# Optimization experiments

Measured on AMD Instinct MI355X. Metric: run time of the kernel, lower is better.

## Reference

```python
import jax, jax.numpy as jnp
import numpy as np

FIELD = 39
VOCAB = 100000
EMB = 32
H1, H2 = 32, 32
BATCH = 16384


def setup_inputs() -> dict:
    key = jax.random.key(0)
    ks = jax.random.split(key, 10)
    Xi = jax.random.randint(ks[0], (BATCH, FIELD, 1), 0, VOCAB, dtype=jnp.int64 if jax.config.read('jax_enable_x64') else jnp.int32)
    Xv = jax.random.uniform(ks[1], (BATCH, FIELD), dtype=jnp.float32)
    # stacked per-field embedding tables (ModuleList of nn.Embedding)
    W1 = jax.random.normal(ks[2], (FIELD, VOCAB, 1), dtype=jnp.float32) * 0.01   # first-order
    W2 = jax.random.normal(ks[3], (FIELD, VOCAB, EMB), dtype=jnp.float32) * 0.01 # second-order
    # deep MLP params (torch Linear: y = x @ W.T + b; stored here as [in, out])
    lin1_w = jax.random.normal(ks[4], (FIELD * EMB, H1), dtype=jnp.float32) * (1.0 / np.sqrt(FIELD * EMB))
    lin1_b = jax.random.normal(ks[5], (H1,), dtype=jnp.float32) * 0.01
    lin2_w = jax.random.normal(ks[6], (H1, H2), dtype=jnp.float32) * (1.0 / np.sqrt(H1))
    lin2_b = jax.random.normal(ks[7], (H2,), dtype=jnp.float32) * 0.01
    bias = jax.random.normal(ks[8], (1,), dtype=jnp.float32)
    return {"Xi": Xi, "Xv": Xv, "W1": W1, "W2": W2, "lin1_w": lin1_w,
            "lin1_b": lin1_b, "lin2_w": lin2_w, "lin2_b": lin2_b, "bias": bias}


def reference(Xi, Xv, W1, W2, lin1_w, lin1_b, lin2_w, lin2_b, bias):
    B, F = Xv.shape
    idx = Xi[:, :, 0]                      # [B, F]
    f_idx = jnp.arange(F)[None, :]         # broadcast over batch
    # fused per-field gather + value scale (replaces the Python loop over 39 tables)
    first = W1[f_idx, idx][..., 0] * Xv            # [B, F]
    second_emb = W2[f_idx, idx] * Xv[:, :, None]   # [B, F, E]
    # FM second order: 0.5 * ((sum e)^2 - sum e^2)
    s = jnp.sum(second_emb, axis=1)                             # [B, E]
    second = 0.5 * (s * s - jnp.sum(second_emb * second_emb, axis=1))  # [B, E]
    # deep part
    deep_emb = second_emb.reshape(B, -1)                        # [B, F*E]
    x = jax.nn.relu(deep_emb @ lin1_w + lin1_b)
    x = jax.nn.relu(x @ lin2_w + lin2_b)
    total = jnp.sum(first, axis=1) + jnp.sum(second, axis=1) + jnp.sum(x, axis=1) + bias
    return total  # [B]
```

## Files before the change

### kernel.cpp

```cpp
#include <hip/hip_runtime.h>
#include <stdint.h>

#define FIELD 39
#define VOCAB 100000
#define EMB   32
#define NH1   32
#define NH2   32
#define NBATCH 16384

typedef __attribute__((ext_vector_type(8))) short short8;
typedef __attribute__((ext_vector_type(4))) float f32x4;
typedef __attribute__((ext_vector_type(4))) unsigned int u32x4;

__device__ __host__ inline unsigned short f2bf(float f) {
    union { float f; unsigned u; } v; v.f = f;
    unsigned r = v.u + 0x7FFF + ((v.u >> 16) & 1);
    return (unsigned short)(r >> 16);
}

__global__ void prep_bpack(const float* __restrict__ lin1_w,
                           unsigned short* __restrict__ bpack) {
    int t = blockIdx.x * 256 + threadIdx.x;
    const int total = FIELD * 2 * 4 * 16 * 8;
    if (t >= total) return;
    int e = t & 7;
    int h = (t >> 3) & 15;
    int g = (t >> 7) & 3;
    int c = (t >> 9) & 1;
    int f = t >> 10;
    int k = f * 32 + 8 * g + e;
    bpack[t] = f2bf(lin1_w[k * 32 + c * 16 + h]);
}

__global__ __launch_bounds__(64)
void deepfm_main(const int* __restrict__ Xi, const float* __restrict__ Xv,
                 const float* __restrict__ W1, const float* __restrict__ W2,
                 const unsigned short* __restrict__ bpack,
                 const float* __restrict__ lin1_b, const float* __restrict__ lin2_w,
                 const float* __restrict__ lin2_b, const float* __restrict__ bias,
                 float* __restrict__ out) {
    __shared__ int   idx_s[16 * FIELD];
    __shared__ float xv_s[16 * FIELD];
    __shared__ __align__(16) float w2_s[NH1 * NH2];
    __shared__ float x_s[16 * 33];

    const int lane = threadIdx.x;
    const int r    = lane & 15;
    const int g    = lane >> 4;
    const int row0 = blockIdx.x * 16;

    for (int i = lane; i < 16 * FIELD; i += 64) {
        idx_s[i] = Xi[row0 * FIELD + i];
        xv_s[i]  = Xv[row0 * FIELD + i];
    }
    for (int i = lane; i < NH1 * NH2; i += 64) w2_s[i] = lin2_w[i];
    __syncthreads();

    f32x4 acc0 = {0.f, 0.f, 0.f, 0.f};
    f32x4 acc1 = {0.f, 0.f, 0.f, 0.f};
    f32x4 sa = {0.f,0.f,0.f,0.f}, sb = {0.f,0.f,0.f,0.f};
    f32x4 qa = {0.f,0.f,0.f,0.f}, qb = {0.f,0.f,0.f,0.f};
    float first = 0.f;

    f32x4 pa0, pa1, pa2, pb0, pb1, pb2;
    u32x4 q00, q01, q02, q10, q11, q12;
    float w1v0, w1v1, w1v2, xvv0, xvv1, xvv2;

#define ISSUE(F, PA, PB, Q0, Q1, WV, XVV) {                              \
        int f_ = (F) < FIELD ? (F) : (FIELD - 1);                        \
        int ii = idx_s[r * FIELD + f_];                                  \
        XVV = xv_s[r * FIELD + f_];                                      \
        const float* w2p = W2 + (size_t)(f_ * VOCAB + ii) * EMB + g * 8; \
        PA = *(const f32x4*)(w2p);                                       \
        PB = *(const f32x4*)(w2p + 4);                                   \
        WV = W1[f_ * VOCAB + ii];                                        \
        const unsigned short* bp = bpack + f_ * 1024 + g * 128 + r * 8;  \
        Q0 = *(const u32x4*)(bp);                                        \
        Q1 = *(const u32x4*)(bp + 512);                                  \
    }

#define COMPUTE(PA, PB, Q0, Q1, WV, XVV) {                               \
        f32x4 ea = PA * XVV;                                             \
        f32x4 eb = PB * XVV;                                             \
        sa += ea; qa += ea * ea;                                         \
        sb += eb; qb += eb * eb;                                         \
        unsigned p0, p1, p2, p3;                                         \
        asm("v_cvt_pk_bf16_f32 %0, %1, %2" : "=v"(p0) : "v"(ea.x), "v"(ea.y)); \
        asm("v_cvt_pk_bf16_f32 %0, %1, %2" : "=v"(p1) : "v"(ea.z), "v"(ea.w)); \
        asm("v_cvt_pk_bf16_f32 %0, %1, %2" : "=v"(p2) : "v"(eb.x), "v"(eb.y)); \
        asm("v_cvt_pk_bf16_f32 %0, %1, %2" : "=v"(p3) : "v"(eb.z), "v"(eb.w)); \
        u32x4 afu = {p0, p1, p2, p3};                                    \
        short8 a8 = __builtin_bit_cast(short8, afu);                     \
        acc0 = __builtin_amdgcn_mfma_f32_16x16x32_bf16(                  \
                   a8, __builtin_bit_cast(short8, Q0), acc0, 0, 0, 0);   \
        acc1 = __builtin_amdgcn_mfma_f32_16x16x32_bf16(                  \
                   a8, __builtin_bit_cast(short8, Q1), acc1, 0, 0, 0);   \
        first += WV * XVV;                                               \
    }

    ISSUE(0, pa0, pb0, q00, q10, w1v0, xvv0);
    ISSUE(1, pa1, pb1, q01, q11, w1v1, xvv1);
    for (int i = 0; i < 13; ++i) {
        int f = 3 * i;
        ISSUE(f + 2, pa2, pb2, q02, q12, w1v2, xvv2);
        COMPUTE(pa0, pb0, q00, q10, w1v0, xvv0);
        ISSUE(f + 3, pa0, pb0, q00, q10, w1v0, xvv0);
        COMPUTE(pa1, pb1, q01, q11, w1v1, xvv1);
        ISSUE(f + 4, pa1, pb1, q01, q11, w1v1, xvv1);
        COMPUTE(pa2, pb2, q02, q12, w1v2, xvv2);
    }
#undef ISSUE
#undef COMPUTE

    float sec = 0.f;
#pragma unroll
    for (int j = 0; j < 4; ++j) {
        sec += 0.5f * (sa[j] * sa[j] - qa[j]);
        sec += 0.5f * (sb[j] * sb[j] - qb[j]);
    }
    sec += __shfl_xor(sec, 16);
    sec += __shfl_xor(sec, 32);

    float b1a = lin1_b[r];
    float b1b = lin1_b[16 + r];
#pragma unroll
    for (int j = 0; j < 4; ++j) {
        int rw = g * 4 + j;
        x_s[rw * 33 + r]      = fmaxf(acc0[j] + b1a, 0.f);
        x_s[rw * 33 + 16 + r] = fmaxf(acc1[j] + b1b, 0.f);
    }
    __syncthreads();

    f32x4 y0 = { lin2_b[g*8+0], lin2_b[g*8+1], lin2_b[g*8+2], lin2_b[g*8+3] };
    f32x4 y1 = { lin2_b[g*8+4], lin2_b[g*8+5], lin2_b[g*8+6], lin2_b[g*8+7] };
#pragma unroll
    for (int h = 0; h < 32; ++h) {
        float xh = x_s[r * 33 + h];
        f32x4 wA = *(const f32x4*)&w2_s[h * 32 + g * 8];
        f32x4 wB = *(const f32x4*)&w2_s[h * 32 + g * 8 + 4];
        y0 += xh * wA;
        y1 += xh * wB;
    }
    float dsum = 0.f;
#pragma unroll
    for (int j = 0; j < 4; ++j) {
        dsum += fmaxf(y0[j], 0.f);
        dsum += fmaxf(y1[j], 0.f);
    }
    dsum += __shfl_xor(dsum, 16);
    dsum += __shfl_xor(dsum, 32);

    if (g == 0) out[row0 + r] = first + sec + dsum + bias[0];
}

extern "C" void kernel_launch(void* const* d_in, const int* in_sizes, int n_in,
                              void* d_out, int out_size, void* d_ws, size_t ws_size,
                              hipStream_t stream) {
    const int*   Xi   = (const int*)d_in[0];
    const float* Xv   = (const float*)d_in[1];
    const float* W1   = (const float*)d_in[2];
    const float* W2   = (const float*)d_in[3];
    const float* l1w  = (const float*)d_in[4];
    const float* l1b  = (const float*)d_in[5];
    const float* l2w  = (const float*)d_in[6];
    const float* l2b  = (const float*)d_in[7];
    const float* bias = (const float*)d_in[8];
    unsigned short* bpack = (unsigned short*)d_ws;

    hipLaunchKernelGGL(prep_bpack, dim3(156), dim3(256), 0, stream, l1w, bpack);
    hipLaunchKernelGGL(deepfm_main, dim3(NBATCH / 16), dim3(64), 0, stream,
                       Xi, Xv, W1, W2, bpack, l1b, l2w, l2b, bias, (float*)d_out);
}
```

Measured before the change: 564.5 us.

## Split field loop across four waves per block with LDS partial-sum reduction

Each 16-row block now runs four wavefronts. Each wave handles every fourth field, so one wave's serial field chain shrinks from 39 to about 10 gathers. Per-wave partial MFMA accumulators, FM sums and first-order sums are written to shared memory and reduced by wave 0, which then runs the small MLP tail. This raises memory-level parallelism for the random embedding gathers, at the cost of extra LDS traffic, more barriers, and three waves idling during the tail.

New measurement: 589.3 us. +4.4%, slower.

```diff
diff --git a/kernel.cpp b/kernel.cpp
--- a/kernel.cpp
+++ b/kernel.cpp
@@ -32,7 +32,7 @@
     bpack[t] = f2bf(lin1_w[k * 32 + c * 16 + h]);
 }
 
-__global__ __launch_bounds__(64)
+__global__ __launch_bounds__(256, 4)
 void deepfm_main(const int* __restrict__ Xi, const float* __restrict__ Xv,
                  const float* __restrict__ W1, const float* __restrict__ W2,
                  const unsigned short* __restrict__ bpack,
@@ -43,17 +43,23 @@
     __shared__ float xv_s[16 * FIELD];
     __shared__ __align__(16) float w2_s[NH1 * NH2];
     __shared__ float x_s[16 * 33];
-
-    const int lane = threadIdx.x;
+    __shared__ __align__(16) float accP[4][64][8];
+    __shared__ __align__(16) float sP[4][64][8];
+    __shared__ __align__(16) float qP[4][64][8];
+    __shared__ float fP[4][64];
+
+    const int tid  = threadIdx.x;
+    const int w    = tid >> 6;
+    const int lane = tid & 63;
     const int r    = lane & 15;
     const int g    = lane >> 4;
     const int row0 = blockIdx.x * 16;
 
-    for (int i = lane; i < 16 * FIELD; i += 64) {
+    for (int i = tid; i < 16 * FIELD; i += 256) {
         idx_s[i] = Xi[row0 * FIELD + i];
         xv_s[i]  = Xv[row0 * FIELD + i];
     }
-    for (int i = lane; i < NH1 * NH2; i += 64) w2_s[i] = lin2_w[i];
+    for (int i = tid; i < NH1 * NH2; i += 256) w2_s[i] = lin2_w[i];
     __syncthreads();
 
     f32x4 acc0 = {0.f, 0.f, 0.f, 0.f};
@@ -66,10 +72,11 @@
     u32x4 q00, q01, q02, q10, q11, q12;
     float w1v0, w1v1, w1v2, xvv0, xvv1, xvv2;
 
-#define ISSUE(F, PA, PB, Q0, Q1, WV, XVV) {                              \
-        int f_ = (F) < FIELD ? (F) : (FIELD - 1);                        \
+#define ISSUE(K, PA, PB, Q0, Q1, WV, XVV) {                              \
+        int F_ = 4 * (K) + w;                                            \
+        int f_ = (F_ < FIELD) ? F_ : (FIELD - 1);                        \
         int ii = idx_s[r * FIELD + f_];                                  \
-        XVV = xv_s[r * FIELD + f_];                                      \
+        XVV = (F_ < FIELD) ? xv_s[r * FIELD + f_] : 0.f;                 \
         const float* w2p = W2 + (size_t)(f_ * VOCAB + ii) * EMB + g * 8; \
         PA = *(const f32x4*)(w2p);                                       \
         PB = *(const f32x4*)(w2p + 4);                                   \
@@ -100,57 +107,93 @@
 
     ISSUE(0, pa0, pb0, q00, q10, w1v0, xvv0);
     ISSUE(1, pa1, pb1, q01, q11, w1v1, xvv1);
-    for (int i = 0; i < 13; ++i) {
-        int f = 3 * i;
-        ISSUE(f + 2, pa2, pb2, q02, q12, w1v2, xvv2);
-        COMPUTE(pa0, pb0, q00, q10, w1v0, xvv0);
-        ISSUE(f + 3, pa0, pb0, q00, q10, w1v0, xvv0);
-        COMPUTE(pa1, pb1, q01, q11, w1v1, xvv1);
-        ISSUE(f + 4, pa1, pb1, q01, q11, w1v1, xvv1);
-        COMPUTE(pa2, pb2, q02, q12, w1v2, xvv2);
-    }
+    ISSUE(2, pa2, pb2, q02, q12, w1v2, xvv2);
+    COMPUTE(pa0, pb0, q00, q10, w1v0, xvv0);
+    ISSUE(3, pa0, pb0, q00, q10, w1v0, xvv0);
+    COMPUTE(pa1, pb1, q01, q11, w1v1, xvv1);
+    ISSUE(4, pa1, pb1, q01, q11, w1v1, xvv1);
+    COMPUTE(pa2, pb2, q02, q12, w1v2, xvv2);
+    ISSUE(5, pa2, pb2, q02, q12, w1v2, xvv2);
+    COMPUTE(pa0, pb0, q00, q10, w1v0, xvv0);
+    ISSUE(6, pa0, pb0, q00, q10, w1v0, xvv0);
+    COMPUTE(pa1, pb1, q01, q11, w1v1, xvv1);
+    ISSUE(7, pa1, pb1, q01, q11, w1v1, xvv1);
+    COMPUTE(pa2, pb2, q02, q12, w1v2, xvv2);
+    ISSUE(8, pa2, pb2, q02, q12, w1v2, xvv2);
+    COMPUTE(pa0, pb0, q00, q10, w1v0, xvv0);
+    ISSUE(9, pa0, pb0, q00, q10, w1v0, xvv0);
+    COMPUTE(pa1, pb1, q01, q11, w1v1, xvv1);
+    COMPUTE(pa2, pb2, q02, q12, w1v2, xvv2);
+    COMPUTE(pa0, pb0, q00, q10, w1v0, xvv0);
 #undef ISSUE
 #undef COMPUTE
 
-    float sec = 0.f;
-#pragma unroll
-    for (int j = 0; j < 4; ++j) {
-        sec += 0.5f * (sa[j] * sa[j] - qa[j]);
-        sec += 0.5f * (sb[j] * sb[j] - qb[j]);
-    }
-    sec += __shfl_xor(sec, 16);
-    sec += __shfl_xor(sec, 32);
-
-    float b1a = lin1_b[r];
-    float b1b = lin1_b[16 + r];
-#pragma unroll
-    for (int j = 0; j < 4; ++j) {
-        int rw = g * 4 + j;
-        x_s[rw * 33 + r]      = fmaxf(acc0[j] + b1a, 0.f);
-        x_s[rw * 33 + 16 + r] = fmaxf(acc1[j] + b1b, 0.f);
-    }
+    *(f32x4*)&accP[w][lane][0] = acc0;
+    *(f32x4*)&accP[w][lane][4] = acc1;
+    *(f32x4*)&sP[w][lane][0]   = sa;
+    *(f32x4*)&sP[w][lane][4]   = sb;
+    *(f32x4*)&qP[w][lane][0]   = qa;
+    *(f32x4*)&qP[w][lane][4]   = qb;
+    fP[w][lane] = first;
     __syncthreads();
 
-    f32x4 y0 = { lin2_b[g*8+0], lin2_b[g*8+1], lin2_b[g*8+2], lin2_b[g*8+3] };
-    f32x4 y1 = { lin2_b[g*8+4], lin2_b[g*8+5], lin2_b[g*8+6], lin2_b[g*8+7] };
-#pragma unroll
-    for (int h = 0; h < 32; ++h) {
-        float xh = x_s[r * 33 + h];
-        f32x4 wA = *(const f32x4*)&w2_s[h * 32 + g * 8];
-        f32x4 wB = *(const f32x4*)&w2_s[h * 32 + g * 8 + 4];
-        y0 += xh * wA;
-        y1 += xh * wB;
-    }
-    float dsum = 0.f;
-#pragma unroll
-    for (int j = 0; j < 4; ++j) {
-        dsum += fmaxf(y0[j], 0.f);
-        dsum += fmaxf(y1[j], 0.f);
-    }
-    dsum += __shfl_xor(dsum, 16);
-    dsum += __shfl_xor(dsum, 32);
-
-    if (g == 0) out[row0 + r] = first + sec + dsum + bias[0];
+    if (w == 0) {
+        acc0 = *(const f32x4*)&accP[0][lane][0] + *(const f32x4*)&accP[1][lane][0]
+             + *(const f32x4*)&accP[2][lane][0] + *(const f32x4*)&accP[3][lane][0];
+        acc1 = *(const f32x4*)&accP[0][lane][4] + *(const f32x4*)&accP[1][lane][4]
+             + *(const f32x4*)&accP[2][lane][4] + *(const f32x4*)&accP[3][lane][4];
+        sa = *(const f32x4*)&sP[0][lane][0] + *(const f32x4*)&sP[1][lane][0]
+           + *(const f32x4*)&sP[2][lane][0] + *(const f32x4*)&sP[3][lane][0];
+        sb = *(const f32x4*)&sP[0][lane][4] + *(const f32x4*)&sP[1][lane][4]
+           + *(const f32x4*)&sP[2][lane][4] + *(const f32x4*)&sP[3][lane][4];
+        qa = *(const f32x4*)&qP[0][lane][0] + *(const f32x4*)&qP[1][lane][0]
+           + *(const f32x4*)&qP[2][lane][0] + *(const f32x4*)&qP[3][lane][0];
+        qb = *(const f32x4*)&qP[0][lane][4] + *(const f32x4*)&qP[1][lane][4]
+           + *(const f32x4*)&qP[2][lane][4] + *(const f32x4*)&qP[3][lane][4];
+        first = fP[0][lane] + fP[1][lane] + fP[2][lane] + fP[3][lane];
+
+        float b1a = lin1_b[r];
+        float b1b = lin1_b[16 + r];
+#pragma unroll
+        for (int j = 0; j < 4; ++j) {
+            int rw = g * 4 + j;
+            x_s[rw * 33 + r]      = fmaxf(acc0[j] + b1a, 0.f);
+            x_s[rw * 33 + 16 + r] = fmaxf(acc1[j] + b1b, 0.f);
+        }
+    }
+    __syncthreads();
+
+    if (w == 0) {
+        float sec = 0.f;
+#pragma unroll
+        for (int j = 0; j < 4; ++j) {
+            sec += 0.5f * (sa[j] * sa[j] - qa[j]);
+            sec += 0.5f * (sb[j] * sb[j] - qb[j]);
+        }
+        sec += __shfl_xor(sec, 16);
+        sec += __shfl_xor(sec, 32);
+
+        f32x4 y0 = { lin2_b[g*8+0], lin2_b[g*8+1], lin2_b[g*8+2], lin2_b[g*8+3] };
+        f32x4 y1 = { lin2_b[g*8+4], lin2_b[g*8+5], lin2_b[g*8+6], lin2_b[g*8+7] };
+#pragma unroll
+        for (int h = 0; h < 32; ++h) {
+            float xh = x_s[r * 33 + h];
+            f32x4 wA = *(const f32x4*)&w2_s[h * 32 + g * 8];
+            f32x4 wB = *(const f32x4*)&w2_s[h * 32 + g * 8 + 4];
+            y0 += xh * wA;
+            y1 += xh * wB;
+        }
+        float dsum = 0.f;
+#pragma unroll
+        for (int j = 0; j < 4; ++j) {
+            dsum += fmaxf(y0[j], 0.f);
+            dsum += fmaxf(y1[j], 0.f);
+        }
+        dsum += __shfl_xor(dsum, 16);
+        dsum += __shfl_xor(dsum, 32);
+
+        if (g == 0) out[row0 + r] = first + sec + dsum + bias[0];
+    }
 }
 
 extern "C" void kernel_launch(void* const* d_in, const int* in_sizes, int n_in,
@@ -168,6 +211,6 @@
     unsigned short* bpack = (unsigned short*)d_ws;
 
     hipLaunchKernelGGL(prep_bpack, dim3(156), dim3(256), 0, stream, l1w, bpack);
-    hipLaunchKernelGGL(deepfm_main, dim3(NBATCH / 16), dim3(64), 0, stream,
+    hipLaunchKernelGGL(deepfm_main, dim3(NBATCH / 16), dim3(256), 0, stream,
                        Xi, Xv, W1, W2, bpack, l1b, l2w, l2b, bias, (float*)d_out);
 }
```
